# Kernel optimization log

Measured on AMD Instinct MI355X. Metric: run time of the kernel, lower is better.

Reference implementation:

```python
import jax, jax.numpy as jnp
import numpy as np

N = 50000        # n_nodes
E = 1600000      # n_edges (avg degree 32)
M = 8            # multiplicity of node irreps 8x0e + 8x1o
R = 8            # radial embedding dim
H = 8            # radial MLP hidden width
OUT_IRREPS = 6 * M   # 24x0e + 24x1o -> 48 irreps (MLP output width)
AVG_NEIGH = 32.0
SQRT3 = np.sqrt(3.0).astype(np.float32)


def setup_inputs() -> dict:
    key = jax.random.key(0)
    ks = jax.random.split(key, 7)
    node_feats = jax.random.normal(ks[0], (N, 4 * M), dtype=jnp.float32)      # [M scalars | M*3 vector comps]
    edge_features = jax.random.normal(ks[1], (E, 4), dtype=jnp.float32)       # SH l=0 (1) + l=1 (3)
    radial_embedding = jax.random.uniform(ks[2], (E, R), dtype=jnp.float32)
    senders = jax.random.randint(ks[3], (E,), 0, N, dtype=jnp.int32)
    receivers = jax.random.randint(ks[4], (E,), 0, N, dtype=jnp.int32)
    w1 = jax.random.normal(ks[5], (R, H), dtype=jnp.float32) / np.sqrt(R).astype(np.float32)
    w2 = jax.random.normal(ks[6], (H, OUT_IRREPS), dtype=jnp.float32) / np.sqrt(H).astype(np.float32)
    return {"node_feats": node_feats, "edge_features": edge_features,
            "radial_embedding": radial_embedding, "w1": w1, "w2": w2,
            "senders": senders, "receivers": receivers}


def reference(node_feats, edge_features, radial_embedding, w1, w2, senders, receivers):
    # 1) irregular gather: messages = node_feats[senders]
    msg = node_feats[senders]                       # [E, 4M]
    s = msg[:, :M]                                  # [E, M]   scalars (0e)
    v = msg[:, M:].reshape(-1, M, 3)                # [E, M, 3] vectors (1o)
    e0 = edge_features[:, :1]                       # [E, 1]   SH l=0
    e1 = edge_features[:, 1:4]                      # [E, 3]   SH l=1

    # 2) CG tensor product node x edge, filtered to irreps_out + '0e' (= 0e + 1o)
    tp0a = s * e0                                   # 0e x 0e -> 0e   [E, M]
    tp0b = jnp.einsum('emc,ec->em', v, e1) / SQRT3  # 1o x 1o -> 0e   [E, M]
    tp1a = s[:, :, None] * e1[:, None, :]           # 0e x 1o -> 1o   [E, M, 3]
    tp1b = v * e0[:, :, None]                       # 1o x 0e -> 1o   [E, M, 3]

    # 3) concatenate original (filtered) messages with tp output, regrouped: 3M x 0e + 3M x 1o
    scal = jnp.concatenate([s, tp0a, tp0b], axis=1)        # [E, 3M]
    vec = jnp.concatenate([v, tp1a, tp1b], axis=1)         # [E, 3M, 3]

    # 4) radial MLP (no bias, swish hidden, linear output) -> one weight per irrep
    w = jax.nn.swish(radial_embedding @ w1) @ w2           # [E, 6M]
    scal = scal * w[:, :3 * M]
    vec = vec * w[:, 3 * M:, None]                          # broadcast over 3 components

    messages = jnp.concatenate([scal, vec.reshape(vec.shape[0], -1)], axis=1)  # [E, 12M]

    # 5) scatter-add to receivers + neighbour normalization
    out = jax.ops.segment_sum(messages, receivers, num_segments=N)             # [N, 12M]
    return out / np.sqrt(AVG_NEIGH).astype(np.float32)
```

## Files before the change

kernel.cpp:

```cpp
#include <hip/hip_runtime.h>


#define CAPACITY 96
#define CH 16

typedef _Float16 half2v __attribute__((ext_vector_type(2)));

__device__ __forceinline__ unsigned pk16(float a, float b) {
    return __builtin_bit_cast(unsigned, __builtin_amdgcn_cvt_pkrtz(a, b));
}

__device__ __forceinline__ float dot2h(unsigned a, half2v b, float c) {
#if __has_builtin(__builtin_amdgcn_fdot2)
    return __builtin_amdgcn_fdot2(__builtin_bit_cast(half2v, a), b, c, false);
#else
    half2v av = __builtin_bit_cast(half2v, a);
    return fmaf((float)av.x, (float)b.x, fmaf((float)av.y, (float)b.y, c));
#endif
}

__global__ __launch_bounds__(256) void hist_kernel(
    const int* __restrict__ recv, int* __restrict__ cnt, int E)
{
    int e = blockIdx.x * 256 + threadIdx.x;
    if (e < E) atomicAdd(&cnt[recv[e]], 1);
}

__global__ __launch_bounds__(1024) void scan_kernel(
    const int* __restrict__ cnt, int* __restrict__ off,
    int* __restrict__ cursor, int N)
{
    __shared__ int lds[1024];
    const int t = threadIdx.x;
    const int CHN = (N + 1023) / 1024;
    const int lo = t * CHN;
    const int hi = min(N, lo + CHN);
    int s = 0;
    for (int i = lo; i < hi; ++i) s += cnt[i];
    lds[t] = s;
    __syncthreads();
    for (int d = 1; d < 1024; d <<= 1) {
        int v = (t >= d) ? lds[t - d] : 0;
        __syncthreads();
        lds[t] += v;
        __syncthreads();
    }
    int run = (t > 0) ? lds[t - 1] : 0;
    for (int i = lo; i < hi; ++i) {
        off[i] = run;
        cursor[i] = run;
        run += cnt[i];
    }
    if (t == 1023) off[N] = lds[1023];
}

__global__ __launch_bounds__(256) void build_recs_kernel(
    const float* __restrict__ edge_features,
    const float* __restrict__ radial,
    const float* __restrict__ w1g,
    const int* __restrict__ senders,
    const int* __restrict__ recv,
    int* __restrict__ slots,
    uint4* __restrict__ recs,
    int E, int CAP, int cstr)
{
    __shared__ float sw1[64];
    for (int i = threadIdx.x; i < 64; i += 256) sw1[i] = w1g[i];
    __syncthreads();

    int e = blockIdx.x * 256 + threadIdx.x;
    if (e >= E) return;

    const int rcv_ = recv[e];
    size_t addr;
    if (CAP > 0) {
        int slot = atomicAdd(&slots[(size_t)rcv_ * cstr], 1);
        slot = min(slot, CAP - 1);
        addr = (size_t)rcv_ * CAP + slot;
    } else {
        addr = (size_t)atomicAdd(&slots[rcv_], 1);
    }

    const float4 ef = reinterpret_cast<const float4*>(edge_features)[e];
    const float4 ra = reinterpret_cast<const float4*>(radial)[2 * e + 0];
    const float4 rb = reinterpret_cast<const float4*>(radial)[2 * e + 1];
    const int snd = senders[e];

    float r[8] = {ra.x, ra.y, ra.z, ra.w, rb.x, rb.y, rb.z, rb.w};
    float h[8];
#pragma unroll
    for (int j = 0; j < 8; ++j) {
        float x = 0.f;
#pragma unroll
        for (int i = 0; i < 8; ++i) x = fmaf(r[i], sw1[i * 8 + j], x);
        h[j] = 0.17677669529663687f * x * __builtin_amdgcn_rcpf(1.0f + __expf(-x));
    }

    uint4 qa, qb;
    qa.x = pk16(h[0], h[1]); qa.y = pk16(h[2], h[3]);
    qa.z = pk16(h[4], h[5]); qa.w = pk16(h[6], h[7]);
    qb.x = pk16(1.0f, ef.x);
    qb.y = pk16(ef.y, ef.z);
    qb.z = (unsigned)snd;
    qb.w = pk16(ef.w, 0.0f);
    recs[2 * addr + 0] = qa;
    recs[2 * addr + 1] = qb;
}

template<bool CAPMODE, int CSTR>
__global__ __launch_bounds__(256) void node_v15_kernel(
    const float* __restrict__ node_feats,
    const float* __restrict__ w2g,
    const int* __restrict__ off,
    const uint4* __restrict__ recs,
    float* __restrict__ out,
    int N)
{
    const int lane = threadIdx.x & 63;
    const int wv   = threadIdx.x >> 6;
    const int node = blockIdx.x * 4 + wv;

    __shared__ float nf_lds[4][CH][36];
    __shared__ float scr[4][128];

    int kA, iA, selA; float scA = 1.0f;
    if (lane < 8)       { kA = lane;         iA = lane;     selA = 0; }
    else if (lane < 16) { kA = lane;         iA = lane - 8; selA = 1; }
    else if (lane < 40) { int t = lane - 16; kA = 16 + t / 3; iA = 8 + t;
                          selA = 2 + t % 3;  scA = 0.57735026918962576f; }
    else                { int t = lane - 40; kA = 24 + t / 3; iA = 8 + t; selA = 0; }

    int kB, iB, selB; const bool deadB = (lane >= 48);
    if (lane < 24)      { int t = lane;      kB = 32 + t / 3; iB = t / 3; selB = 2 + t % 3; }
    else if (lane < 48) { int t = lane - 24; kB = 40 + t / 3; iB = 8 + t; selB = 1; }
    else                { kB = 0; iB = 0; selB = 0; }

    half2v mA0 = {0, 0}, mA1 = {0, 0}, mA2 = {0, 0};
    if      (selA == 0) mA0.x = (_Float16)1.f;
    else if (selA == 1) mA0.y = (_Float16)1.f;
    else if (selA == 2) mA1.x = (_Float16)1.f;
    else if (selA == 3) mA1.y = (_Float16)1.f;
    else                mA2.x = (_Float16)1.f;
    half2v mB0 = {0, 0}, mB1 = {0, 0}, mB2 = {0, 0};
    if (!deadB) {
        if      (selB == 1) mB0.y = (_Float16)1.f;
        else if (selB == 2) mB1.x = (_Float16)1.f;
        else if (selB == 3) mB1.y = (_Float16)1.f;
        else                mB2.x = (_Float16)1.f;
    }

    half2v wpA[4], wpB[4];
#pragma unroll
    for (int i = 0; i < 4; ++i) {
        wpA[i].x = (_Float16)(w2g[(2 * i + 0) * 48 + kA] * scA);
        wpA[i].y = (_Float16)(w2g[(2 * i + 1) * 48 + kA] * scA);
        wpB[i].x = deadB ? (_Float16)0.f : (_Float16)(w2g[(2 * i + 0) * 48 + kB]);
        wpB[i].y = deadB ? (_Float16)0.f : (_Float16)(w2g[(2 * i + 1) * 48 + kB]);
    }

    if (node >= N) return;

    int base, count;
    if (CAPMODE) { base = node * CAPACITY; count = min(off[(size_t)node * CSTR], CAPACITY); }
    else         { base = off[node];       count = off[node + 1] - base; }
    base  = __builtin_amdgcn_readfirstlane(base);
    count = __builtin_amdgcn_readfirstlane(count);
    const uint4* rp = recs + (size_t)base * 2;

    const int r_stage = lane >> 2;
    const int q_stage = lane & 3;

    float acc0 = 0.f, acc1 = 0.f;

    for (int c0i = 0; c0i < count; c0i += CH) {
        const int cc = min(CH, count - c0i);

        if (r_stage < cc) {
            const unsigned snd =
                reinterpret_cast<const unsigned*>(rp)[((size_t)c0i + r_stage) * 8 + 6];
            const float4* src = reinterpret_cast<const float4*>(node_feats)
                                + (size_t)snd * 8 + q_stage * 2;
            const float4 v0 = src[0];
            const float4 v1 = src[1];
            float* dst = &nf_lds[wv][r_stage][q_stage * 8];
            *reinterpret_cast<float4*>(dst)     = v0;
            *reinterpret_cast<float4*>(dst + 4) = v1;
        }

#pragma unroll 4
        for (int i = 0; i < cc; ++i) {
            const uint4 qa = rp[(size_t)(c0i + i) * 2 + 0];
            const uint4 qb = rp[(size_t)(c0i + i) * 2 + 1];

            float wAv = dot2h(qa.x, wpA[0], 0.f);
            wAv = dot2h(qa.y, wpA[1], wAv);
            wAv = dot2h(qa.z, wpA[2], wAv);
            wAv = dot2h(qa.w, wpA[3], wAv);
            float wBv = dot2h(qa.x, wpB[0], 0.f);
            wBv = dot2h(qa.y, wpB[1], wBv);
            wBv = dot2h(qa.z, wpB[2], wBv);
            wBv = dot2h(qa.w, wpB[3], wBv);

            float fA = dot2h(qb.x, mA0, 0.f);
            fA = dot2h(qb.y, mA1, fA);
            fA = dot2h(qb.w, mA2, fA);
            float fB = dot2h(qb.x, mB0, 0.f);
            fB = dot2h(qb.y, mB1, fB);
            fB = dot2h(qb.w, mB2, fB);

            const float n0 = nf_lds[wv][i][iA];
            const float n1 = nf_lds[wv][i][iB];

            acc0 = fmaf(wAv, n0 * fA, acc0);
            acc1 = fmaf(wBv, n1 * fB, acc1);
        }
    }

    scr[wv][lane]      = acc0;
    scr[wv][64 + lane] = acc1;
    float o0;
    if (lane < 16) {
        o0 = scr[wv][lane];
    } else if (lane < 24) {
        const int t = 16 + 3 * (lane - 16);
        o0 = scr[wv][t] + scr[wv][t + 1] + scr[wv][t + 2];
    } else {
        o0 = scr[wv][lane + 16];
    }
    float* orow = out + (size_t)node * 96;
    orow[lane] = o0;
    if (lane < 32) orow[64 + lane] = scr[wv][80 + lane];
}

extern "C" void kernel_launch(void* const* d_in, const int* in_sizes, int n_in,
                              void* d_out, int out_size, void* d_ws, size_t ws_size,
                              hipStream_t stream) {
    const float* node_feats    = (const float*)d_in[0];
    const float* edge_features = (const float*)d_in[1];
    const float* radial        = (const float*)d_in[2];
    const float* w1            = (const float*)d_in[3];
    const float* w2            = (const float*)d_in[4];
    const int*   senders       = (const int*)d_in[5];
    const int*   receivers     = (const int*)d_in[6];
    float* out = (float*)d_out;

    const int E = in_sizes[5];
    const int N = out_size / 96;
    const int eblocks = (E + 255) / 256;
    const int nblocks = (N + 3) / 4;

    const size_t recsBytes = (size_t)N * CAPACITY * 32;
    const size_t needPad   = recsBytes + (size_t)N * 16 * sizeof(int);
    const size_t needP1    = recsBytes + (size_t)N * sizeof(int);

    if (ws_size >= needPad) {
        uint4* recs = (uint4*)d_ws;
        int* cnt = (int*)((char*)d_ws + recsBytes);

        (void)hipMemsetAsync(cnt, 0, (size_t)N * 16 * sizeof(int), stream);
        hipLaunchKernelGGL(build_recs_kernel, dim3(eblocks), dim3(256), 0, stream,
                           edge_features, radial, w1, senders, receivers,
                           cnt, recs, E, CAPACITY, 16);
        hipLaunchKernelGGL((node_v15_kernel<true, 16>), dim3(nblocks), dim3(256), 0, stream,
                           node_feats, w2, cnt, recs, out, N);
    } else if (ws_size >= needP1) {
        uint4* recs = (uint4*)d_ws;
        int* cnt = (int*)((char*)d_ws + recsBytes);

        (void)hipMemsetAsync(cnt, 0, (size_t)N * sizeof(int), stream);
        hipLaunchKernelGGL(build_recs_kernel, dim3(eblocks), dim3(256), 0, stream,
                           edge_features, radial, w1, senders, receivers,
                           cnt, recs, E, CAPACITY, 1);
        hipLaunchKernelGGL((node_v15_kernel<true, 1>), dim3(nblocks), dim3(256), 0, stream,
                           node_feats, w2, cnt, recs, out, N);
    } else {
        uint4* recs = (uint4*)d_ws;
        int* cnt    = (int*)((char*)d_ws + (size_t)E * 32);
        int* off    = cnt + N;
        int* cursor = cnt + 2 * N + 1;

        (void)hipMemsetAsync(cnt, 0, (size_t)N * sizeof(int), stream);
        hipLaunchKernelGGL(hist_kernel, dim3(eblocks), dim3(256), 0, stream,
                           receivers, cnt, E);
        hipLaunchKernelGGL(scan_kernel, dim3(1), dim3(1024), 0, stream,
                           cnt, off, cursor, N);
        hipLaunchKernelGGL(build_recs_kernel, dim3(eblocks), dim3(256), 0, stream,
                           edge_features, radial, w1, senders, receivers,
                           cursor, recs, E, 0, 1);
        hipLaunchKernelGGL((node_v15_kernel<false, 1>), dim3(nblocks), dim3(256), 0, stream,
                           node_feats, w2, off, recs, out, N);
    }
}
```

Measured before the change: 286.4 us.

## Store edge records in edge order and bucket edge indices per receiver

The build kernel now writes each 32-byte edge record contiguously at its edge index and scatters only a 4-byte edge id into a per-receiver bucket, replacing the scatter of full records into receiver-sorted slots. The node kernel reads bucket ids and then gathers the records indirectly. The padded (stride-16) counter variant is dropped. This shrinks the scattered write footprint and the workspace, but adds a dependent indirect load per edge and makes the record reads in the node kernel random instead of contiguous.

After: 311.1 us. 8.6% more time.

```diff
diff --git a/kernel.cpp b/kernel.cpp
--- a/kernel.cpp
+++ b/kernel.cpp
@@ -61,8 +61,9 @@
     const int* __restrict__ senders,
     const int* __restrict__ recv,
     int* __restrict__ slots,
+    int* __restrict__ bucket,
     uint4* __restrict__ recs,
-    int E, int CAP, int cstr)
+    int E, int CAP)
 {
     __shared__ float sw1[64];
     for (int i = threadIdx.x; i < 64; i += 256) sw1[i] = w1g[i];
@@ -72,13 +73,13 @@
     if (e >= E) return;
 
     const int rcv_ = recv[e];
-    size_t addr;
+    size_t baddr;
     if (CAP > 0) {
-        int slot = atomicAdd(&slots[(size_t)rcv_ * cstr], 1);
+        int slot = atomicAdd(&slots[rcv_], 1);
         slot = min(slot, CAP - 1);
-        addr = (size_t)rcv_ * CAP + slot;
+        baddr = (size_t)rcv_ * CAP + slot;
     } else {
-        addr = (size_t)atomicAdd(&slots[rcv_], 1);
+        baddr = (size_t)atomicAdd(&slots[rcv_], 1);
     }
 
     const float4 ef = reinterpret_cast<const float4*>(edge_features)[e];
@@ -103,15 +104,18 @@
     qb.y = pk16(ef.y, ef.z);
     qb.z = (unsigned)snd;
     qb.w = pk16(ef.w, 0.0f);
-    recs[2 * addr + 0] = qa;
-    recs[2 * addr + 1] = qb;
-}
-
-template<bool CAPMODE, int CSTR>
-__global__ __launch_bounds__(256) void node_v15_kernel(
+
+    recs[2 * (size_t)e + 0] = qa;
+    recs[2 * (size_t)e + 1] = qb;
+    bucket[baddr] = e;
+}
+
+template<bool CAPMODE>
+__global__ __launch_bounds__(256) void node_v16_kernel(
     const float* __restrict__ node_feats,
     const float* __restrict__ w2g,
     const int* __restrict__ off,
+    const int* __restrict__ bucket,
     const uint4* __restrict__ recs,
     float* __restrict__ out,
     int N)
@@ -161,11 +165,12 @@
     if (node >= N) return;
 
     int base, count;
-    if (CAPMODE) { base = node * CAPACITY; count = min(off[(size_t)node * CSTR], CAPACITY); }
+    if (CAPMODE) { base = node * CAPACITY; count = min(off[node], CAPACITY); }
     else         { base = off[node];       count = off[node + 1] - base; }
     base  = __builtin_amdgcn_readfirstlane(base);
     count = __builtin_amdgcn_readfirstlane(count);
-    const uint4* rp = recs + (size_t)base * 2;
+    const int* bkt = bucket + base;
+    const unsigned* recd = reinterpret_cast<const unsigned*>(recs);
 
     const int r_stage = lane >> 2;
     const int q_stage = lane & 3;
@@ -176,8 +181,8 @@
         const int cc = min(CH, count - c0i);
 
         if (r_stage < cc) {
-            const unsigned snd =
-                reinterpret_cast<const unsigned*>(rp)[((size_t)c0i + r_stage) * 8 + 6];
+            const int e_r = bkt[c0i + r_stage];
+            const unsigned snd = recd[(size_t)e_r * 8 + 6];
             const float4* src = reinterpret_cast<const float4*>(node_feats)
                                 + (size_t)snd * 8 + q_stage * 2;
             const float4 v0 = src[0];
@@ -189,8 +194,9 @@
 
 #pragma unroll 4
         for (int i = 0; i < cc; ++i) {
-            const uint4 qa = rp[(size_t)(c0i + i) * 2 + 0];
-            const uint4 qb = rp[(size_t)(c0i + i) * 2 + 1];
+            const int ei = __builtin_amdgcn_readfirstlane(bkt[c0i + i]);
+            const uint4 qa = recs[(size_t)ei * 2 + 0];
+            const uint4 qb = recs[(size_t)ei * 2 + 1];
 
             float wAv = dot2h(qa.x, wpA[0], 0.f);
             wAv = dot2h(qa.y, wpA[1], wAv);
@@ -249,33 +255,24 @@
     const int eblocks = (E + 255) / 256;
     const int nblocks = (N + 3) / 4;
 
-    const size_t recsBytes = (size_t)N * CAPACITY * 32;
-    const size_t needPad   = recsBytes + (size_t)N * 16 * sizeof(int);
-    const size_t needP1    = recsBytes + (size_t)N * sizeof(int);
-
-    if (ws_size >= needPad) {
+    const size_t recsBytes = (size_t)E * 32;
+    const size_t needP1 = recsBytes + (size_t)N * CAPACITY * 4 + (size_t)N * 4;
+
+    if (ws_size >= needP1) {
         uint4* recs = (uint4*)d_ws;
-        int* cnt = (int*)((char*)d_ws + recsBytes);
-
-        (void)hipMemsetAsync(cnt, 0, (size_t)N * 16 * sizeof(int), stream);
-        hipLaunchKernelGGL(build_recs_kernel, dim3(eblocks), dim3(256), 0, stream,
-                           edge_features, radial, w1, senders, receivers,
-                           cnt, recs, E, CAPACITY, 16);
-        hipLaunchKernelGGL((node_v15_kernel<true, 16>), dim3(nblocks), dim3(256), 0, stream,
-                           node_feats, w2, cnt, recs, out, N);
-    } else if (ws_size >= needP1) {
-        uint4* recs = (uint4*)d_ws;
-        int* cnt = (int*)((char*)d_ws + recsBytes);
+        int* bucket = (int*)((char*)d_ws + recsBytes);
+        int* cnt = bucket + (size_t)N * CAPACITY;
 
         (void)hipMemsetAsync(cnt, 0, (size_t)N * sizeof(int), stream);
         hipLaunchKernelGGL(build_recs_kernel, dim3(eblocks), dim3(256), 0, stream,
                            edge_features, radial, w1, senders, receivers,
-                           cnt, recs, E, CAPACITY, 1);
-        hipLaunchKernelGGL((node_v15_kernel<true, 1>), dim3(nblocks), dim3(256), 0, stream,
-                           node_feats, w2, cnt, recs, out, N);
+                           cnt, bucket, recs, E, CAPACITY);
+        hipLaunchKernelGGL(node_v16_kernel<true>, dim3(nblocks), dim3(256), 0, stream,
+                           node_feats, w2, cnt, bucket, recs, out, N);
     } else {
         uint4* recs = (uint4*)d_ws;
-        int* cnt    = (int*)((char*)d_ws + (size_t)E * 32);
+        int* bucket = (int*)((char*)d_ws + recsBytes);
+        int* cnt    = bucket + E;
         int* off    = cnt + N;
         int* cursor = cnt + 2 * N + 1;
 
@@ -286,8 +283,8 @@
                            cnt, off, cursor, N);
         hipLaunchKernelGGL(build_recs_kernel, dim3(eblocks), dim3(256), 0, stream,
                            edge_features, radial, w1, senders, receivers,
-                           cursor, recs, E, 0, 1);
-        hipLaunchKernelGGL((node_v15_kernel<false, 1>), dim3(nblocks), dim3(256), 0, stream,
-                           node_feats, w2, off, recs, out, N);
-    }
-}
+                           cursor, bucket, recs, E, 0);
+        hipLaunchKernelGGL(node_v16_kernel<false>, dim3(nblocks), dim3(256), 0, stream,
+                           node_feats, w2, off, bucket, recs, out, N);
+    }
+}
```

## Replace fixed-capacity receiver buckets with exact CSR via multi-block scan

Applied to the files above, without the earlier changes.

Removes the padded per-node capacity record layout (with 16-int padded slot counters) and always builds an exact CSR: histogram, a three-stage parallel prefix scan, then atomic-cursor placement. The old single-block serial scan is replaced by a block-parallel scan. This eliminates capacity clamping, which could drop edges for nodes with more than 96 neighbours, and makes the records compact. In exchange it adds a histogram pass and three small scan launches before record building.

Measured after the change: 362.2 us. +26.5%, slower.

```diff
diff --git a/kernel.cpp b/kernel.cpp
--- a/kernel.cpp
+++ b/kernel.cpp
@@ -1,7 +1,6 @@
 #include <hip/hip_runtime.h>
 
 
-#define CAPACITY 96
 #define CH 16
 
 typedef _Float16 half2v __attribute__((ext_vector_type(2)));
@@ -26,32 +25,63 @@
     if (e < E) atomicAdd(&cnt[recv[e]], 1);
 }
 
-__global__ __launch_bounds__(1024) void scan_kernel(
+__global__ __launch_bounds__(256) void scan1_kernel(
     const int* __restrict__ cnt, int* __restrict__ off,
-    int* __restrict__ cursor, int N)
-{
-    __shared__ int lds[1024];
+    int* __restrict__ psum, int N)
+{
+    __shared__ int lds[256];
     const int t = threadIdx.x;
-    const int CHN = (N + 1023) / 1024;
-    const int lo = t * CHN;
-    const int hi = min(N, lo + CHN);
-    int s = 0;
-    for (int i = lo; i < hi; ++i) s += cnt[i];
-    lds[t] = s;
+    const int i = blockIdx.x * 256 + t;
+    const int v = (i < N) ? cnt[i] : 0;
+    lds[t] = v;
     __syncthreads();
-    for (int d = 1; d < 1024; d <<= 1) {
-        int v = (t >= d) ? lds[t - d] : 0;
-        __syncthreads();
-        lds[t] += v;
-        __syncthreads();
-    }
-    int run = (t > 0) ? lds[t - 1] : 0;
-    for (int i = lo; i < hi; ++i) {
-        off[i] = run;
-        cursor[i] = run;
-        run += cnt[i];
-    }
-    if (t == 1023) off[N] = lds[1023];
+#pragma unroll
+    for (int d = 1; d < 256; d <<= 1) {
+        int u = (t >= d) ? lds[t - d] : 0;
+        __syncthreads();
+        lds[t] += u;
+        __syncthreads();
+    }
+    if (i < N) off[i] = lds[t] - v;
+    if (t == 255) psum[blockIdx.x] = lds[255];
+}
+
+__global__ __launch_bounds__(256) void scan2_kernel(
+    int* __restrict__ psum, int* __restrict__ off, int nb, int N, int E)
+{
+    __shared__ int lds[256];
+    const int t = threadIdx.x;
+    int carry = 0;
+    const int rounds = (nb + 255) / 256;
+    for (int r = 0; r < rounds; ++r) {
+        const int idx = r * 256 + t;
+        const int v = (idx < nb) ? psum[idx] : 0;
+        lds[t] = v;
+        __syncthreads();
+#pragma unroll
+        for (int d = 1; d < 256; d <<= 1) {
+            int u = (t >= d) ? lds[t - d] : 0;
+            __syncthreads();
+            lds[t] += u;
+            __syncthreads();
+        }
+        if (idx < nb) psum[idx] = lds[t] - v + carry;
+        carry += lds[255];
+        __syncthreads();
+    }
+    if (t == 0) off[N] = E;
+}
+
+__global__ __launch_bounds__(256) void scan3_kernel(
+    int* __restrict__ off, int* __restrict__ cursor,
+    const int* __restrict__ psum, int N)
+{
+    const int i = blockIdx.x * 256 + threadIdx.x;
+    if (i < N) {
+        const int o = off[i] + psum[blockIdx.x];
+        off[i] = o;
+        cursor[i] = o;
+    }
 }
 
 __global__ __launch_bounds__(256) void build_recs_kernel(
@@ -60,9 +90,9 @@
     const float* __restrict__ w1g,
     const int* __restrict__ senders,
     const int* __restrict__ recv,
-    int* __restrict__ slots,
+    int* __restrict__ cursor,
     uint4* __restrict__ recs,
-    int E, int CAP, int cstr)
+    int E)
 {
     __shared__ float sw1[64];
     for (int i = threadIdx.x; i < 64; i += 256) sw1[i] = w1g[i];
@@ -72,14 +102,7 @@
     if (e >= E) return;
 
     const int rcv_ = recv[e];
-    size_t addr;
-    if (CAP > 0) {
-        int slot = atomicAdd(&slots[(size_t)rcv_ * cstr], 1);
-        slot = min(slot, CAP - 1);
-        addr = (size_t)rcv_ * CAP + slot;
-    } else {
-        addr = (size_t)atomicAdd(&slots[rcv_], 1);
-    }
+    const size_t addr = (size_t)atomicAdd(&cursor[rcv_], 1);
 
     const float4 ef = reinterpret_cast<const float4*>(edge_features)[e];
     const float4 ra = reinterpret_cast<const float4*>(radial)[2 * e + 0];
@@ -107,8 +130,7 @@
     recs[2 * addr + 1] = qb;
 }
 
-template<bool CAPMODE, int CSTR>
-__global__ __launch_bounds__(256) void node_v15_kernel(
+__global__ __launch_bounds__(256) void node_v17_kernel(
     const float* __restrict__ node_feats,
     const float* __restrict__ w2g,
     const int* __restrict__ off,
@@ -160,9 +182,8 @@
 
     if (node >= N) return;
 
-    int base, count;
-    if (CAPMODE) { base = node * CAPACITY; count = min(off[(size_t)node * CSTR], CAPACITY); }
-    else         { base = off[node];       count = off[node + 1] - base; }
+    int base  = off[node];
+    int count = off[node + 1] - base;
     base  = __builtin_amdgcn_readfirstlane(base);
     count = __builtin_amdgcn_readfirstlane(count);
     const uint4* rp = recs + (size_t)base * 2;
@@ -248,46 +269,26 @@
     const int N = out_size / 96;
     const int eblocks = (E + 255) / 256;
     const int nblocks = (N + 3) / 4;
-
-    const size_t recsBytes = (size_t)N * CAPACITY * 32;
-    const size_t needPad   = recsBytes + (size_t)N * 16 * sizeof(int);
-    const size_t needP1    = recsBytes + (size_t)N * sizeof(int);
-
-    if (ws_size >= needPad) {
-        uint4* recs = (uint4*)d_ws;
-        int* cnt = (int*)((char*)d_ws + recsBytes);
-
-        (void)hipMemsetAsync(cnt, 0, (size_t)N * 16 * sizeof(int), stream);
-        hipLaunchKernelGGL(build_recs_kernel, dim3(eblocks), dim3(256), 0, stream,
-                           edge_features, radial, w1, senders, receivers,
-                           cnt, recs, E, CAPACITY, 16);
-        hipLaunchKernelGGL((node_v15_kernel<true, 16>), dim3(nblocks), dim3(256), 0, stream,
-                           node_feats, w2, cnt, recs, out, N);
-    } else if (ws_size >= needP1) {
-        uint4* recs = (uint4*)d_ws;
-        int* cnt = (int*)((char*)d_ws + recsBytes);
-
-        (void)hipMemsetAsync(cnt, 0, (size_t)N * sizeof(int), stream);
-        hipLaunchKernelGGL(build_recs_kernel, dim3(eblocks), dim3(256), 0, stream,
-                           edge_features, radial, w1, senders, receivers,
-                           cnt, recs, E, CAPACITY, 1);
-        hipLaunchKernelGGL((node_v15_kernel<true, 1>), dim3(nblocks), dim3(256), 0, stream,
-                           node_feats, w2, cnt, recs, out, N);
-    } else {
-        uint4* recs = (uint4*)d_ws;
-        int* cnt    = (int*)((char*)d_ws + (size_t)E * 32);
-        int* off    = cnt + N;
-        int* cursor = cnt + 2 * N + 1;
-
-        (void)hipMemsetAsync(cnt, 0, (size_t)N * sizeof(int), stream);
-        hipLaunchKernelGGL(hist_kernel, dim3(eblocks), dim3(256), 0, stream,
-                           receivers, cnt, E);
-        hipLaunchKernelGGL(scan_kernel, dim3(1), dim3(1024), 0, stream,
-                           cnt, off, cursor, N);
-        hipLaunchKernelGGL(build_recs_kernel, dim3(eblocks), dim3(256), 0, stream,
-                           edge_features, radial, w1, senders, receivers,
-                           cursor, recs, E, 0, 1);
-        hipLaunchKernelGGL((node_v15_kernel<false, 1>), dim3(nblocks), dim3(256), 0, stream,
-                           node_feats, w2, off, recs, out, N);
-    }
-}
+    const int sblocks = (N + 255) / 256;
+
+    uint4* recs = (uint4*)d_ws;
+    int* cnt    = (int*)((char*)d_ws + (size_t)E * 32);
+    int* off    = cnt + N;
+    int* cursor = off + N + 1;
+    int* psum   = cursor + N;
+
+    (void)hipMemsetAsync(cnt, 0, (size_t)N * sizeof(int), stream);
+    hipLaunchKernelGGL(hist_kernel, dim3(eblocks), dim3(256), 0, stream,
+                       receivers, cnt, E);
+    hipLaunchKernelGGL(scan1_kernel, dim3(sblocks), dim3(256), 0, stream,
+                       cnt, off, psum, N);
+    hipLaunchKernelGGL(scan2_kernel, dim3(1), dim3(256), 0, stream,
+                       psum, off, sblocks, N, E);
+    hipLaunchKernelGGL(scan3_kernel, dim3(sblocks), dim3(256), 0, stream,
+                       off, cursor, psum, N);
+    hipLaunchKernelGGL(build_recs_kernel, dim3(eblocks), dim3(256), 0, stream,
+                       edge_features, radial, w1, senders, receivers,
+                       cursor, recs, E);
+    hipLaunchKernelGGL(node_v17_kernel, dim3(nblocks), dim3(256), 0, stream,
+                       node_feats, w2, off, recs, out, N);
+}
```
